# Performance work log

Measured on AMD Instinct MI355X. Metric: run time of the kernel, lower is better.

Reference implementation:

```python
import jax, jax.numpy as jnp
import numpy as np

N, C, K = 8192, 512, 64


def setup_inputs() -> dict:
    key = jax.random.key(0)
    k1, k2, k3 = jax.random.split(key, 3)
    return {
        "f_i": jax.random.normal(k1, (N, C), dtype=jnp.float32),
        "f_j": jax.random.normal(k2, (N, C), dtype=jnp.float32),
        "means": jax.random.normal(k3, (K, C), dtype=jnp.float32),
        "scales": jnp.ones((K, C), dtype=jnp.float32),
        "weights": jnp.ones((K,), dtype=jnp.float32),
    }


def _neg_sq_dist(f, means, scales):
    # f: [N, C], means/scales: [K, C] -> [N, K]
    d = (f[:, None, :] - means[None, :, :]) / scales[None, :, :]
    return -jnp.sum(d * d, axis=-1)


def reference(f_i, f_j, means, scales, weights):
    # Original: kernel[n,m,k] = exp(dist_i[n,k] + dist_j[m,k]); out = kernel @ weights.
    # This factors exactly as (exp(dist_i) * w) @ exp(dist_j)^T, avoiding the
    # O(N*N*K) intermediate while computing identical math.
    dist_i = _neg_sq_dist(f_i, means, scales)  # [N, K]
    dist_j = _neg_sq_dist(f_j, means, scales)  # [N, K]
    phi_i = jnp.exp(dist_i) * weights[None, :]  # [N, K]
    phi_j = jnp.exp(dist_j)                      # [N, K]
    return phi_i @ phi_j.T                       # [N, N]
```

## Files before the change

### kernel.cpp

```cpp
#include <hip/hip_runtime.h>
#include <math.h>

#define NP   8192
#define CD   512
#define KD   64
#define TWON 16384

__global__ __launch_bounds__(256) void prep_kernel(
    const float* __restrict__ means, const float* __restrict__ scales,
    float* __restrict__ VT, float* __restrict__ cst)
{
    const int k = blockIdx.x;
    const int t = threadIdx.x;
    __shared__ float red[256];
    float local = 0.f;
    for (int c = t; c < CD; c += 256) {
        float m    = means[k * CD + c];
        float s    = scales[k * CD + c];
        float inv  = 1.0f / s;
        float inv2 = inv * inv;
        VT[c * KD + k]        = 2.0f * m * inv2;
        VT[(CD + c) * KD + k] = -inv2;
        local += m * m * inv2;
    }
    red[t] = local;
    __syncthreads();
    for (int off = 128; off > 0; off >>= 1) {
        if (t < off) red[t] += red[t + off];
        __syncthreads();
    }
    if (t == 0) cst[k] = red[0];
}

__global__ __launch_bounds__(256) void phi_kernel(
    const float* __restrict__ f_i, const float* __restrict__ f_j,
    const float* __restrict__ VT, const float* __restrict__ cst,
    const float* __restrict__ weights, float* __restrict__ phiT)
{
    __shared__ float Us[64 * 33];
    __shared__ float Vs[64 * 68];
    const int t  = threadIdx.x;
    const int n0 = blockIdx.x * 32;
    const bool iside = (n0 < NP);
    const float* f = iside ? (f_i + (size_t)n0 * CD)
                           : (f_j + (size_t)(n0 - NP) * CD);

    const int k0 = (t & 15) * 4;
    const int r0 = (t >> 4) * 2;
    float acc[2][4] = {};

    for (int ch = 0; ch < 16; ++ch) {
        const int gc = ch * 64;
        const bool sq = (ch >= 8);
        const int fc = sq ? (gc - CD) : gc;

        #pragma unroll
        for (int j = 0; j < 2; ++j) {
            int v   = t + j * 256;
            int row = v >> 4;
            int c4  = (v & 15) * 4;
            float4 val = *(const float4*)(f + (size_t)row * CD + fc + c4);
            if (sq) { val.x *= val.x; val.y *= val.y; val.z *= val.z; val.w *= val.w; }
            Us[(c4 + 0) * 33 + row] = val.x;
            Us[(c4 + 1) * 33 + row] = val.y;
            Us[(c4 + 2) * 33 + row] = val.z;
            Us[(c4 + 3) * 33 + row] = val.w;
        }
        #pragma unroll
        for (int j = 0; j < 4; ++j) {
            int v  = t + j * 256;
            int cc = v >> 4;
            int k4 = (v & 15) * 4;
            float4 val = *(const float4*)(VT + (size_t)(gc + cc) * KD + k4);
            *(float4*)&Vs[cc * 68 + k4] = val;
        }
        __syncthreads();

        #pragma unroll 8
        for (int cc = 0; cc < 64; ++cc) {
            float a0 = Us[cc * 33 + r0];
            float a1 = Us[cc * 33 + r0 + 1];
            float4 b = *(const float4*)&Vs[cc * 68 + k0];
            acc[0][0] += a0 * b.x; acc[0][1] += a0 * b.y;
            acc[0][2] += a0 * b.z; acc[0][3] += a0 * b.w;
            acc[1][0] += a1 * b.x; acc[1][1] += a1 * b.y;
            acc[1][2] += a1 * b.z; acc[1][3] += a1 * b.w;
        }
        __syncthreads();
    }

    const float4 cst4 = *(const float4*)&cst[k0];
    float4 wv4 = make_float4(1.f, 1.f, 1.f, 1.f);
    if (iside) wv4 = *(const float4*)&weights[k0];
    const float cs[4] = {cst4.x, cst4.y, cst4.z, cst4.w};
    const float wv[4] = {wv4.x, wv4.y, wv4.z, wv4.w};
    #pragma unroll
    for (int r = 0; r < 2; ++r) {
        #pragma unroll
        for (int kj = 0; kj < 4; ++kj) {
            float ph = expf(acc[r][kj] - cs[kj]) * wv[kj];
            phiT[(size_t)(k0 + kj) * TWON + n0 + r0 + r] = ph;
        }
    }
}

__global__ __launch_bounds__(256) void gemm_kernel(
    const float* __restrict__ phiT, float* __restrict__ out)
{
    __shared__ float As[64 * 128];
    __shared__ float Bs[64 * 128];
    const int t  = threadIdx.x;
    const int rb = blockIdx.y * 128;
    const int cb = blockIdx.x * 128;

    #pragma unroll
    for (int j = 0; j < 8; ++j) {
        int v = t + j * 256;
        int k = v >> 5;
        int r = (v & 31) * 4;
        *(float4*)&As[k * 128 + r] =
            *(const float4*)&phiT[(size_t)k * TWON + rb + r];
        *(float4*)&Bs[k * 128 + r] =
            *(const float4*)&phiT[(size_t)k * TWON + NP + cb + r];
    }
    __syncthreads();

    const int c0 = (t & 15) * 8;
    const int r0 = (t >> 4) * 8;
    float acc[8][8] = {};

    #pragma unroll 8
    for (int k = 0; k < 64; ++k) {
        float4 a0 = *(const float4*)&As[k * 128 + r0];
        float4 a1 = *(const float4*)&As[k * 128 + r0 + 4];
        float4 b0 = *(const float4*)&Bs[k * 128 + c0];
        float4 b1 = *(const float4*)&Bs[k * 128 + c0 + 4];
        float a[8] = {a0.x, a0.y, a0.z, a0.w, a1.x, a1.y, a1.z, a1.w};
        float b[8] = {b0.x, b0.y, b0.z, b0.w, b1.x, b1.y, b1.z, b1.w};
        #pragma unroll
        for (int ri = 0; ri < 8; ++ri)
            #pragma unroll
            for (int cj = 0; cj < 8; ++cj)
                acc[ri][cj] += a[ri] * b[cj];
    }

    #pragma unroll
    for (int ri = 0; ri < 8; ++ri) {
        size_t row = (size_t)(rb + r0 + ri);
        float4* o = (float4*)&out[row * NP + cb + c0];
        o[0] = make_float4(acc[ri][0], acc[ri][1], acc[ri][2], acc[ri][3]);
        o[1] = make_float4(acc[ri][4], acc[ri][5], acc[ri][6], acc[ri][7]);
    }
}

extern "C" void kernel_launch(void* const* d_in, const int* in_sizes, int n_in,
                              void* d_out, int out_size, void* d_ws, size_t ws_size,
                              hipStream_t stream) {
    const float* f_i     = (const float*)d_in[0];
    const float* f_j     = (const float*)d_in[1];
    const float* means   = (const float*)d_in[2];
    const float* scales  = (const float*)d_in[3];
    const float* weights = (const float*)d_in[4];
    float* out = (float*)d_out;

    float* ws   = (float*)d_ws;
    float* VT   = ws;
    float* cst  = ws + 65536;
    float* phiT = ws + 65600;

    prep_kernel<<<64, 256, 0, stream>>>(means, scales, VT, cst);
    phi_kernel<<<512, 256, 0, stream>>>(f_i, f_j, VT, cst, weights, phiT);
    gemm_kernel<<<dim3(64, 64), 256, 0, stream>>>(phiT, out);
}
```

Before: 372.5 us.

## Use bf16 MFMA for the final GEMM and fuse squaring in phi kernel

The phi kernel now writes phi row-major in bf16 and processes 64 rows per block. It computes the linear and squared terms in one pass over each f chunk, so f is loaded once instead of twice. The output GEMM drops the FP32 shared-memory outer-product loop for bf16 MFMA 16x16x32 instructions, loading operands straight from global memory into registers. This targets the compute cost of the K=64 GEMM over an 8192x8192 output. The trade-off is that phi values are rounded to bf16 before the product, which lowers precision, and the output stores are scattered per element rather than vectorised.

Result: faster. 357.3 us (-4.1%).

```diff
diff --git a/kernel.cpp b/kernel.cpp
--- a/kernel.cpp
+++ b/kernel.cpp
@@ -1,10 +1,14 @@
 #include <hip/hip_runtime.h>
+#include <hip/hip_bf16.h>
 #include <math.h>
 
 #define NP   8192
 #define CD   512
 #define KD   64
 #define TWON 16384
+
+typedef __attribute__((ext_vector_type(8))) short short8;
+typedef __attribute__((ext_vector_type(4))) float f32x4;
 
 __global__ __launch_bounds__(256) void prep_kernel(
     const float* __restrict__ means, const float* __restrict__ scales,
@@ -35,122 +39,136 @@
 __global__ __launch_bounds__(256) void phi_kernel(
     const float* __restrict__ f_i, const float* __restrict__ f_j,
     const float* __restrict__ VT, const float* __restrict__ cst,
-    const float* __restrict__ weights, float* __restrict__ phiT)
+    const float* __restrict__ weights, __hip_bfloat16* __restrict__ phi)
 {
-    __shared__ float Us[64 * 33];
-    __shared__ float Vs[64 * 68];
+    __shared__ float Us [64 * 68];
+    __shared__ float Vs1[64 * 68];
+    __shared__ float Vs2[64 * 68];
     const int t  = threadIdx.x;
-    const int n0 = blockIdx.x * 32;
+    const int n0 = blockIdx.x * 64;
     const bool iside = (n0 < NP);
     const float* f = iside ? (f_i + (size_t)n0 * CD)
                            : (f_j + (size_t)(n0 - NP) * CD);
 
-    const int k0 = (t & 15) * 4;
-    const int r0 = (t >> 4) * 2;
-    float acc[2][4] = {};
+    const int k0 = (t & 7) * 8;
+    const int rg = t >> 3;
+    float acc[2][8] = {};
 
-    for (int ch = 0; ch < 16; ++ch) {
-        const int gc = ch * 64;
-        const bool sq = (ch >= 8);
-        const int fc = sq ? (gc - CD) : gc;
-
+    for (int ch = 0; ch < 8; ++ch) {
+        const int c0 = ch * 64;
         #pragma unroll
-        for (int j = 0; j < 2; ++j) {
+        for (int j = 0; j < 4; ++j) {
             int v   = t + j * 256;
             int row = v >> 4;
             int c4  = (v & 15) * 4;
-            float4 val = *(const float4*)(f + (size_t)row * CD + fc + c4);
-            if (sq) { val.x *= val.x; val.y *= val.y; val.z *= val.z; val.w *= val.w; }
-            Us[(c4 + 0) * 33 + row] = val.x;
-            Us[(c4 + 1) * 33 + row] = val.y;
-            Us[(c4 + 2) * 33 + row] = val.z;
-            Us[(c4 + 3) * 33 + row] = val.w;
-        }
-        #pragma unroll
-        for (int j = 0; j < 4; ++j) {
-            int v  = t + j * 256;
-            int cc = v >> 4;
-            int k4 = (v & 15) * 4;
-            float4 val = *(const float4*)(VT + (size_t)(gc + cc) * KD + k4);
-            *(float4*)&Vs[cc * 68 + k4] = val;
+            *(float4*)&Us[row * 68 + c4] =
+                *(const float4*)&f[(size_t)row * CD + c0 + c4];
+            *(float4*)&Vs1[row * 68 + c4] =
+                *(const float4*)&VT[(size_t)(c0 + row) * KD + c4];
+            *(float4*)&Vs2[row * 68 + c4] =
+                *(const float4*)&VT[(size_t)(CD + c0 + row) * KD + c4];
         }
         __syncthreads();
 
         #pragma unroll 8
         for (int cc = 0; cc < 64; ++cc) {
-            float a0 = Us[cc * 33 + r0];
-            float a1 = Us[cc * 33 + r0 + 1];
-            float4 b = *(const float4*)&Vs[cc * 68 + k0];
-            acc[0][0] += a0 * b.x; acc[0][1] += a0 * b.y;
-            acc[0][2] += a0 * b.z; acc[0][3] += a0 * b.w;
-            acc[1][0] += a1 * b.x; acc[1][1] += a1 * b.y;
-            acc[1][2] += a1 * b.z; acc[1][3] += a1 * b.w;
+            float a0 = Us[rg * 68 + cc];
+            float a1 = Us[(rg + 32) * 68 + cc];
+            float s0 = a0 * a0, s1 = a1 * a1;
+            float4 b1a = *(const float4*)&Vs1[cc * 68 + k0];
+            float4 b1b = *(const float4*)&Vs1[cc * 68 + k0 + 4];
+            float4 b2a = *(const float4*)&Vs2[cc * 68 + k0];
+            float4 b2b = *(const float4*)&Vs2[cc * 68 + k0 + 4];
+            acc[0][0] += a0 * b1a.x + s0 * b2a.x;
+            acc[0][1] += a0 * b1a.y + s0 * b2a.y;
+            acc[0][2] += a0 * b1a.z + s0 * b2a.z;
+            acc[0][3] += a0 * b1a.w + s0 * b2a.w;
+            acc[0][4] += a0 * b1b.x + s0 * b2b.x;
+            acc[0][5] += a0 * b1b.y + s0 * b2b.y;
+            acc[0][6] += a0 * b1b.z + s0 * b2b.z;
+            acc[0][7] += a0 * b1b.w + s0 * b2b.w;
+            acc[1][0] += a1 * b1a.x + s1 * b2a.x;
+            acc[1][1] += a1 * b1a.y + s1 * b2a.y;
+            acc[1][2] += a1 * b1a.z + s1 * b2a.z;
+            acc[1][3] += a1 * b1a.w + s1 * b2a.w;
+            acc[1][4] += a1 * b1b.x + s1 * b2b.x;
+            acc[1][5] += a1 * b1b.y + s1 * b2b.y;
+            acc[1][6] += a1 * b1b.z + s1 * b2b.z;
+            acc[1][7] += a1 * b1b.w + s1 * b2b.w;
         }
         __syncthreads();
     }
 
-    const float4 cst4 = *(const float4*)&cst[k0];
-    float4 wv4 = make_float4(1.f, 1.f, 1.f, 1.f);
-    if (iside) wv4 = *(const float4*)&weights[k0];
-    const float cs[4] = {cst4.x, cst4.y, cst4.z, cst4.w};
-    const float wv[4] = {wv4.x, wv4.y, wv4.z, wv4.w};
+    float cs[8], wv[8];
+    *(float4*)&cs[0] = *(const float4*)&cst[k0];
+    *(float4*)&cs[4] = *(const float4*)&cst[k0 + 4];
+    if (iside) {
+        *(float4*)&wv[0] = *(const float4*)&weights[k0];
+        *(float4*)&wv[4] = *(const float4*)&weights[k0 + 4];
+    } else {
+        #pragma unroll
+        for (int j = 0; j < 8; ++j) wv[j] = 1.0f;
+    }
     #pragma unroll
     for (int r = 0; r < 2; ++r) {
+        int row = n0 + rg + r * 32;
+        union { short8 v; __hip_bfloat16 h[8]; } o;
         #pragma unroll
-        for (int kj = 0; kj < 4; ++kj) {
-            float ph = expf(acc[r][kj] - cs[kj]) * wv[kj];
-            phiT[(size_t)(k0 + kj) * TWON + n0 + r0 + r] = ph;
+        for (int j = 0; j < 8; ++j) {
+            float ph = expf(acc[r][j] - cs[j]) * wv[j];
+            o.h[j] = __float2bfloat16(ph);
         }
+        *(short8*)&phi[(size_t)row * KD + k0] = o.v;
     }
 }
 
 __global__ __launch_bounds__(256) void gemm_kernel(
-    const float* __restrict__ phiT, float* __restrict__ out)
+    const __hip_bfloat16* __restrict__ phi, float* __restrict__ out)
 {
-    __shared__ float As[64 * 128];
-    __shared__ float Bs[64 * 128];
-    const int t  = threadIdx.x;
-    const int rb = blockIdx.y * 128;
-    const int cb = blockIdx.x * 128;
+    const int t    = threadIdx.x;
+    const int lane = t & 63, wave = t >> 6;
+    const int m    = lane & 15, q = lane >> 4;
+    const int i0   = blockIdx.y * 128 + (wave & 1) * 64;
+    const int j0   = blockIdx.x * 128 + (wave >> 1) * 64;
+    const short* phiS = (const short*)phi;
+
+    short8 A[4][2], B[4][2];
+    #pragma unroll
+    for (int it = 0; it < 4; ++it)
+        #pragma unroll
+        for (int kh = 0; kh < 2; ++kh) {
+            A[it][kh] = *(const short8*)
+                &phiS[(size_t)(i0 + it * 16 + m) * KD + kh * 32 + q * 8];
+            B[it][kh] = *(const short8*)
+                &phiS[(size_t)(NP + j0 + it * 16 + m) * KD + kh * 32 + q * 8];
+        }
+
+    f32x4 acc[4][4];
+    #pragma unroll
+    for (int it = 0; it < 4; ++it)
+        #pragma unroll
+        for (int jt = 0; jt < 4; ++jt)
+            acc[it][jt] = (f32x4){0.f, 0.f, 0.f, 0.f};
 
     #pragma unroll
-    for (int j = 0; j < 8; ++j) {
-        int v = t + j * 256;
-        int k = v >> 5;
-        int r = (v & 31) * 4;
-        *(float4*)&As[k * 128 + r] =
-            *(const float4*)&phiT[(size_t)k * TWON + rb + r];
-        *(float4*)&Bs[k * 128 + r] =
-            *(const float4*)&phiT[(size_t)k * TWON + NP + cb + r];
-    }
-    __syncthreads();
-
-    const int c0 = (t & 15) * 8;
-    const int r0 = (t >> 4) * 8;
-    float acc[8][8] = {};
-
-    #pragma unroll 8
-    for (int k = 0; k < 64; ++k) {
-        float4 a0 = *(const float4*)&As[k * 128 + r0];
-        float4 a1 = *(const float4*)&As[k * 128 + r0 + 4];
-        float4 b0 = *(const float4*)&Bs[k * 128 + c0];
-        float4 b1 = *(const float4*)&Bs[k * 128 + c0 + 4];
-        float a[8] = {a0.x, a0.y, a0.z, a0.w, a1.x, a1.y, a1.z, a1.w};
-        float b[8] = {b0.x, b0.y, b0.z, b0.w, b1.x, b1.y, b1.z, b1.w};
+    for (int it = 0; it < 4; ++it)
         #pragma unroll
-        for (int ri = 0; ri < 8; ++ri)
-            #pragma unroll
-            for (int cj = 0; cj < 8; ++cj)
-                acc[ri][cj] += a[ri] * b[cj];
-    }
+        for (int jt = 0; jt < 4; ++jt) {
+            acc[it][jt] = __builtin_amdgcn_mfma_f32_16x16x32_bf16(
+                A[it][0], B[jt][0], acc[it][jt], 0, 0, 0);
+            acc[it][jt] = __builtin_amdgcn_mfma_f32_16x16x32_bf16(
+                A[it][1], B[jt][1], acc[it][jt], 0, 0, 0);
+        }
 
     #pragma unroll
-    for (int ri = 0; ri < 8; ++ri) {
-        size_t row = (size_t)(rb + r0 + ri);
-        float4* o = (float4*)&out[row * NP + cb + c0];
-        o[0] = make_float4(acc[ri][0], acc[ri][1], acc[ri][2], acc[ri][3]);
-        o[1] = make_float4(acc[ri][4], acc[ri][5], acc[ri][6], acc[ri][7]);
-    }
+    for (int it = 0; it < 4; ++it)
+        #pragma unroll
+        for (int r = 0; r < 4; ++r) {
+            size_t row = (size_t)(i0 + it * 16 + q * 4 + r);
+            #pragma unroll
+            for (int jt = 0; jt < 4; ++jt)
+                out[row * NP + j0 + jt * 16 + m] = acc[it][jt][r];
+        }
 }
 
 extern "C" void kernel_launch(void* const* d_in, const int* in_sizes, int n_in,
@@ -166,9 +184,9 @@
     float* ws   = (float*)d_ws;
     float* VT   = ws;
     float* cst  = ws + 65536;
-    float* phiT = ws + 65600;
+    __hip_bfloat16* phi = (__hip_bfloat16*)(ws + 65600);
 
     prep_kernel<<<64, 256, 0, stream>>>(means, scales, VT, cst);
-    phi_kernel<<<512, 256, 0, stream>>>(f_i, f_j, VT, cst, weights, phiT);
-    gemm_kernel<<<dim3(64, 64), 256, 0, stream>>>(phiT, out);
+    phi_kernel<<<256, 256, 0, stream>>>(f_i, f_j, VT, cst, weights, phi);
+    gemm_kernel<<<dim3(64, 64), 256, 0, stream>>>(phi, out);
 }
```
